# Kernel optimization log

Measured on AMD Instinct MI355X. Metric: run time of the kernel, lower is better.

## Reference

```python
import jax, jax.numpy as jnp
import numpy as np

N_NODES = 100000
N_EDGES = 1000000
IN_F = 64
HEADS = 4
OUT_C = 32  # per-head channels
EDGE_DIM = 16
NEG_SLOPE = 0.2


def setup_inputs() -> dict:
    key = jax.random.key(0)
    ks = jax.random.split(key, 10)
    x = jax.random.normal(ks[0], (N_NODES, IN_F), dtype=jnp.float32)
    edge_index = jax.random.randint(ks[1], (2, N_EDGES), 0, N_NODES, dtype=jnp.int64)
    edge_attr = jax.random.normal(ks[2], (N_EDGES, EDGE_DIM), dtype=jnp.float32)
    s = 1.0 / np.sqrt(IN_F)
    W = jax.random.normal(ks[3], (IN_F, HEADS * OUT_C), dtype=jnp.float32) * s
    W_edge = jax.random.normal(ks[4], (EDGE_DIM, HEADS * OUT_C), dtype=jnp.float32) * (1.0 / np.sqrt(EDGE_DIM))
    att_src = jax.random.normal(ks[5], (HEADS, OUT_C), dtype=jnp.float32) * (1.0 / np.sqrt(OUT_C))
    att_dst = jax.random.normal(ks[6], (HEADS, OUT_C), dtype=jnp.float32) * (1.0 / np.sqrt(OUT_C))
    att_edge = jax.random.normal(ks[7], (HEADS, OUT_C), dtype=jnp.float32) * (1.0 / np.sqrt(OUT_C))
    bias = jnp.zeros((HEADS * OUT_C,), dtype=jnp.float32)
    return {"x": x, "edge_index": edge_index, "edge_attr": edge_attr,
            "W": W, "W_edge": W_edge, "att_src": att_src, "att_dst": att_dst,
            "att_edge": att_edge, "bias": bias}


def reference(x, edge_index, edge_attr, W, W_edge, att_src, att_dst, att_edge, bias):
    # PyG GATConv with edge_dim, add_self_loops=False, concat=True.
    N = x.shape[0]
    src = edge_index[0]  # message source j
    dst = edge_index[1]  # message target i

    x_proj = (x @ W).reshape(N, HEADS, OUT_C)          # [N,H,C]
    a_src = jnp.einsum('nhc,hc->nh', x_proj, att_src)  # [N,H]
    a_dst = jnp.einsum('nhc,hc->nh', x_proj, att_dst)  # [N,H]

    e_proj = (edge_attr @ W_edge).reshape(-1, HEADS, OUT_C)  # [E,H,C]
    a_edge = jnp.einsum('ehc,hc->eh', e_proj, att_edge)      # [E,H]

    alpha = a_src[src] + a_dst[dst] + a_edge                 # [E,H]
    alpha = jax.nn.leaky_relu(alpha, NEG_SLOPE)

    # edge softmax grouped by destination node
    seg_max = jax.ops.segment_max(alpha, dst, num_segments=N)  # [N,H]
    alpha = jnp.exp(alpha - seg_max[dst])
    denom = jax.ops.segment_sum(alpha, dst, num_segments=N)    # [N,H]
    alpha = alpha / (denom[dst] + 1e-16)

    msg = x_proj[src] * alpha[:, :, None]                      # [E,H,C]
    out = jax.ops.segment_sum(msg, dst, num_segments=N)        # [N,H,C]
    return out.reshape(N, HEADS * OUT_C) + bias
```

## Files before the change

### kernel.cpp

```cpp
#include <hip/hip_runtime.h>
#include <hip/hip_fp16.h>


#define HC 128
#define NEG 0.2f
#define CH 16
#define DEGS 32
#define K_SHIFT 6.0f

typedef __fp16 half2_t __attribute__((ext_vector_type(2)));

__device__ __forceinline__ unsigned short f2bf(float f) {
    unsigned u = __float_as_uint(f);
    return (unsigned short)((u + 0x7fffu + ((u >> 16) & 1u)) >> 16);
}
__device__ __forceinline__ unsigned pk_h2(float lo, float hi) {
    half2_t p = __builtin_amdgcn_cvt_pkrtz(lo, hi);
    union { half2_t h; unsigned u; } cv;
    cv.h = p;
    return cv.u;
}
__device__ __forceinline__ float h2f_bits(unsigned short bits) {
    __half_raw hr; hr.x = bits;
    return __half2float(*reinterpret_cast<__half*>(&hr));
}
__device__ __forceinline__ long ld_idx(const int* __restrict__ ei, long i, int m64) {
    return m64 ? (long)(((const long long*)ei)[i]) : (long)ei[i];
}
__device__ __forceinline__ int detect_m64(const int* __restrict__ ei, int* s_m64) {
    int t = threadIdx.x;
    if (t < 64) {
        unsigned long long bal = __ballot(ei[2 * t + 1] != 0);
        if (t == 0) *s_m64 = (bal == 0ull) ? 1 : 0;
    }
    __syncthreads();
    return *s_m64;
}

__global__ __launch_bounds__(256) void k_hist(
    const float* __restrict__ We, const float* __restrict__ ae,
    const float* __restrict__ eattr, const int* __restrict__ ei,
    int* __restrict__ deg, int* __restrict__ rank, uint2* __restrict__ aeh,
    int E) {
    __shared__ float q_s[64];
    __shared__ int s_m64;
    int t = threadIdx.x;
    int m64 = detect_m64(ei, &s_m64);
    if (t < 64) {
        int dd = t >> 2, h = t & 3;
        float s = 0.f;
        for (int c = 0; c < 32; ++c)
            s += We[dd * HC + h * 32 + c] * ae[h * 32 + c];
        q_s[t] = s;
    }
    __syncthreads();

    int base = blockIdx.x * 512 + t;
    int e0 = base, e1 = base + 256;
    bool v0 = e0 < E, v1 = e1 < E;

    long d0 = 0, d1 = 0;
    if (v0) d0 = ld_idx(ei, (long)E + e0, m64);
    if (v1) d1 = ld_idx(ei, (long)E + e1, m64);
    int r0 = 0, r1 = 0;
    if (v0) r0 = atomicAdd(&deg[d0 * DEGS], 1);
    if (v1) r1 = atomicAdd(&deg[d1 * DEGS], 1);

#pragma unroll
    for (int k = 0; k < 2; ++k) {
        int e = k ? e1 : e0;
        bool v = k ? v1 : v0;
        if (!v) continue;
        const float4* pe = reinterpret_cast<const float4*>(eattr + (long)e * 16);
        float4 ea0 = pe[0], ea1 = pe[1], ea2 = pe[2], ea3 = pe[3];
        float ev[16] = {ea0.x, ea0.y, ea0.z, ea0.w, ea1.x, ea1.y, ea1.z, ea1.w,
                        ea2.x, ea2.y, ea2.z, ea2.w, ea3.x, ea3.y, ea3.z, ea3.w};
        float ov[4];
#pragma unroll
        for (int h = 0; h < 4; ++h) {
            float aev = 0.f;
#pragma unroll
            for (int dd = 0; dd < 16; ++dd) aev += ev[dd] * q_s[dd * 4 + h];
            ov[h] = aev;
        }
        aeh[e] = make_uint2(pk_h2(ov[0], ov[1]), pk_h2(ov[2], ov[3]));
        rank[e] = k ? r1 : r0;
    }
}

__global__ __launch_bounds__(256) void k_proj(
    const float* __restrict__ x, const float* __restrict__ W,
    const float* __restrict__ as_, const float* __restrict__ ad_,
    unsigned short* __restrict__ xp, float* __restrict__ a_src,
    float* __restrict__ a_dst, int N) {
    __shared__ float x_s[64][68];
    int t = threadIdx.x;
    int n0 = blockIdx.x * 64;
#pragma unroll
    for (int i = 0; i < 4; ++i) {
        int fl = i * 256 + t;
        int node = fl >> 4, f4 = fl & 15;
        float4 v = make_float4(0.f, 0.f, 0.f, 0.f);
        if (n0 + node < N)
            v = *reinterpret_cast<const float4*>(&x[(long)(n0 + node) * 64 + f4 * 4]);
        x_s[f4 * 4 + 0][node] = v.x;
        x_s[f4 * 4 + 1][node] = v.y;
        x_s[f4 * 4 + 2][node] = v.z;
        x_s[f4 * 4 + 3][node] = v.w;
    }
    __syncthreads();

    int c = t & 31;
    int nd = t >> 5;
    const float4* __restrict__ W4 = reinterpret_cast<const float4*>(W);
    float acc[8][4];
#pragma unroll
    for (int i = 0; i < 8; ++i)
#pragma unroll
        for (int j = 0; j < 4; ++j) acc[i][j] = 0.f;

#pragma unroll 8
    for (int k = 0; k < 64; ++k) {
        float4 w4 = W4[k * 32 + c];
        float4 xa = *reinterpret_cast<const float4*>(&x_s[k][nd * 8]);
        float4 xb = *reinterpret_cast<const float4*>(&x_s[k][nd * 8 + 4]);
        float xv[8] = {xa.x, xa.y, xa.z, xa.w, xb.x, xb.y, xb.z, xb.w};
#pragma unroll
        for (int i = 0; i < 8; ++i) {
            acc[i][0] += xv[i] * w4.x;
            acc[i][1] += xv[i] * w4.y;
            acc[i][2] += xv[i] * w4.z;
            acc[i][3] += xv[i] * w4.w;
        }
    }

    float4 s4 = *reinterpret_cast<const float4*>(&as_[c * 4]);
    float4 d4 = *reinterpret_cast<const float4*>(&ad_[c * 4]);
#pragma unroll
    for (int i = 0; i < 8; ++i) {
        int node = n0 + nd * 8 + i;
        if (node < N) {
            ushort4 o;
            o.x = f2bf(acc[i][0]); o.y = f2bf(acc[i][1]);
            o.z = f2bf(acc[i][2]); o.w = f2bf(acc[i][3]);
            *reinterpret_cast<ushort4*>(&xp[(long)node * HC + c * 4]) = o;
        }
        float ps = acc[i][0] * s4.x + acc[i][1] * s4.y + acc[i][2] * s4.z + acc[i][3] * s4.w;
        float pd = acc[i][0] * d4.x + acc[i][1] * d4.y + acc[i][2] * d4.z + acc[i][3] * d4.w;
#pragma unroll
        for (int off = 1; off < 8; off <<= 1) {
            ps += __shfl_xor(ps, off, 64);
            pd += __shfl_xor(pd, off, 64);
        }
        if ((c & 7) == 0 && node < N) {
            int h = c >> 3;
            a_src[(long)node * 4 + h] = ps;
            a_dst[(long)node * 4 + h] = pd;
        }
    }
}

__global__ __launch_bounds__(256) void k_scan1(
    const int* __restrict__ deg, int* __restrict__ row, int* __restrict__ bsum,
    int N) {
    __shared__ int s[256];
    int b = blockIdx.x, t = threadIdx.x;
    int base = b * 1024 + t * 4;
    int v[4], sum = 0;
#pragma unroll
    for (int i = 0; i < 4; ++i) {
        int idx = base + i;
        v[i] = (idx < N) ? deg[(long)idx * DEGS] : 0;
        sum += v[i];
    }
    s[t] = sum;
    __syncthreads();
    for (int off = 1; off < 256; off <<= 1) {
        int xv = (t >= off) ? s[t - off] : 0;
        __syncthreads();
        s[t] += xv;
        __syncthreads();
    }
    int run = s[t] - sum;
#pragma unroll
    for (int i = 0; i < 4; ++i) {
        int idx = base + i;
        if (idx < N) row[idx] = run;
        run += v[i];
    }
    if (t == 255) bsum[b] = s[255];
}

__global__ void k_scan2(int* __restrict__ bsum, int nb) {
    int t = threadIdx.x;
    if (t >= 64) return;
    int i0 = 2 * t, i1 = 2 * t + 1;
    int v0 = (i0 < nb) ? bsum[i0] : 0;
    int v1 = (i1 < nb) ? bsum[i1] : 0;
    int s = v0 + v1;
#pragma unroll
    for (int off = 1; off < 64; off <<= 1) {
        int u = __shfl_up(s, off, 64);
        if (t >= off) s += u;
    }
    int ex = s - (v0 + v1);
    if (i0 < nb) bsum[i0] = ex;
    if (i1 < nb) bsum[i1] = ex + v0;
}

__global__ __launch_bounds__(256) void k_place(
    const int* __restrict__ ei, const uint2* __restrict__ aeh,
    const int* __restrict__ rank, const float* __restrict__ a_src,
    const float* __restrict__ a_dst, const int* __restrict__ row,
    const int* __restrict__ bsum, uint4* __restrict__ srt, int E) {
    __shared__ int s_m64;
    int m64 = detect_m64(ei, &s_m64);
    int base = blockIdx.x * 512 + threadIdx.x;
#pragma unroll
    for (int k = 0; k < 2; ++k) {
        int e = base + k * 256;
        if (e >= E) continue;
        long s = ld_idx(ei, e, m64);
        long d = ld_idx(ei, (long)E + e, m64);
        uint2 av = aeh[e];
        int r = rank[e];
        float4 s4 = *reinterpret_cast<const float4*>(a_src + s * 4);
        float4 d4 = *reinterpret_cast<const float4*>(a_dst + d * 4);
        float lf[4];
        lf[0] = s4.x + d4.x + h2f_bits((unsigned short)(av.x & 0xffffu));
        lf[1] = s4.y + d4.y + h2f_bits((unsigned short)(av.x >> 16));
        lf[2] = s4.z + d4.z + h2f_bits((unsigned short)(av.y & 0xffffu));
        lf[3] = s4.w + d4.w + h2f_bits((unsigned short)(av.y >> 16));
        float ex[4];
#pragma unroll
        for (int h = 0; h < 4; ++h) {
            float v = (lf[h] > 0.f) ? lf[h] : NEG * lf[h];
            ex[h] = __expf(v - K_SHIFT);
        }
        int pos = row[d] + bsum[(int)(d >> 10)] + r;
        srt[pos] = make_uint4((unsigned)s, pk_h2(ex[0], ex[1]),
                              pk_h2(ex[2], ex[3]), 0u);
    }
}

__global__ __launch_bounds__(128) void k_gather(
    const int* __restrict__ row, const int* __restrict__ bsum,
    const uint4* __restrict__ srt, const char* __restrict__ xpc,
    const float* __restrict__ bias, float* __restrict__ out, int N, int E) {
    int wid = threadIdx.x >> 6;
    int lane = threadIdx.x & 63;
    int n = blockIdx.x * 2 + wid;
    if (n >= N) return;
    int beg = row[n] + bsum[n >> 10];
    int end = (n + 1 < N) ? (row[n + 1] + bsum[(n + 1) >> 10]) : E;
    int h_s = lane & 3, e_s = lane >> 2;
    int par = lane >> 5;
    int cl = lane & 31;
    int h_a = cl >> 3;
    float l = 0.f;
    float acc[4] = {0.f, 0.f, 0.f, 0.f};

    __shared__ float s_ex[2][CH][4];
    __shared__ int s_off[2][CH];
    __shared__ float s_l[2][4];

    for (int cs = beg; cs < end; cs += CH) {
        int cnt = end - cs;
        if (cnt > CH) cnt = CH;
        float ex = 0.f;
        if (e_s < cnt) {
            uint4 r = srt[cs + e_s];
            if (h_s == 0) s_off[wid][e_s] = (int)(r.x << 8);
            unsigned pr = (h_s & 2) ? r.z : r.y;
            unsigned bits = (h_s & 1) ? (pr >> 16) : (pr & 0xffffu);
            ex = h2f_bits((unsigned short)bits);
        }
        s_ex[wid][e_s][h_s] = ex;
        float se = ex;
        se += __shfl_xor(se, 4, 64);
        se += __shfl_xor(se, 8, 64);
        se += __shfl_xor(se, 16, 64);
        se += __shfl_xor(se, 32, 64);
        l += se;
        int j = 0;
        for (; j + 4 <= cnt; j += 4) {
            int ea0 = j + par, ea1 = j + 2 + par;
            int o0 = s_off[wid][ea0], o1 = s_off[wid][ea1];
            float w0 = s_ex[wid][ea0][h_a], w1 = s_ex[wid][ea1][h_a];
            uint2 v0 = *reinterpret_cast<const uint2*>(xpc + o0 + cl * 8);
            uint2 v1 = *reinterpret_cast<const uint2*>(xpc + o1 + cl * 8);
            acc[0] += w0 * __uint_as_float(v0.x << 16);
            acc[1] += w0 * __uint_as_float(v0.x & 0xffff0000u);
            acc[2] += w0 * __uint_as_float(v0.y << 16);
            acc[3] += w0 * __uint_as_float(v0.y & 0xffff0000u);
            acc[0] += w1 * __uint_as_float(v1.x << 16);
            acc[1] += w1 * __uint_as_float(v1.x & 0xffff0000u);
            acc[2] += w1 * __uint_as_float(v1.y << 16);
            acc[3] += w1 * __uint_as_float(v1.y & 0xffff0000u);
        }
        for (; j < cnt; j += 2) {
            int e = j + par;
            bool act = e < cnt;
            int o = s_off[wid][act ? e : j];
            float w = act ? s_ex[wid][e][h_a] : 0.f;
            uint2 v = *reinterpret_cast<const uint2*>(xpc + o + cl * 8);
            acc[0] += w * __uint_as_float(v.x << 16);
            acc[1] += w * __uint_as_float(v.x & 0xffff0000u);
            acc[2] += w * __uint_as_float(v.y << 16);
            acc[3] += w * __uint_as_float(v.y & 0xffff0000u);
        }
    }
    if (lane < 4) s_l[wid][h_s] = l;
#pragma unroll
    for (int k = 0; k < 4; ++k) acc[k] += __shfl_xor(acc[k], 32, 64);
    if (par == 0) {
        float d = s_l[wid][h_a] + 1e-16f;
        float4 b4 = *reinterpret_cast<const float4*>(bias + cl * 4);
        float4 o;
        o.x = acc[0] / d + b4.x;
        o.y = acc[1] / d + b4.y;
        o.z = acc[2] / d + b4.z;
        o.w = acc[3] / d + b4.w;
        *reinterpret_cast<float4*>(out + (long)n * HC + cl * 4) = o;
    }
}

extern "C" void kernel_launch(void* const* d_in, const int* in_sizes, int n_in,
                              void* d_out, int out_size, void* d_ws, size_t ws_size,
                              hipStream_t stream) {
    const float* x    = (const float*)d_in[0];
    const int*   ei   = (const int*)d_in[1];
    const float* ea   = (const float*)d_in[2];
    const float* W    = (const float*)d_in[3];
    const float* We   = (const float*)d_in[4];
    const float* as_  = (const float*)d_in[5];
    const float* ad_  = (const float*)d_in[6];
    const float* ae   = (const float*)d_in[7];
    const float* bias = (const float*)d_in[8];
    float* out = (float*)d_out;

    int N = in_sizes[0] / 64;
    int E = in_sizes[1] / 2;

    char* ws = (char*)d_ws;
    size_t off = 0;
    auto take = [&](size_t bytes) -> char* {
        char* p = ws + off;
        off += (bytes + 511) & ~(size_t)511;
        return p;
    };
    unsigned short* xp = (unsigned short*)take((size_t)N * HC * 2);
    float* a_src   = (float*)take((size_t)N * 4 * 4);
    float* a_dst   = (float*)take((size_t)N * 4 * 4);
    uint4* srt     = (uint4*)take((size_t)E * 16);
    uint2* aeh     = (uint2*)take((size_t)E * 8);
    int* rank      = (int*)take((size_t)E * 4);
    int* row       = (int*)take((size_t)(N + 1) * 4);
    int* bsum      = (int*)take(4096 * 4);
    int* deg = (int*)srt;

    int Np = (N + 63) / 64;
    int nblk = (N + 1023) / 1024;

    (void)hipMemsetAsync(deg, 0, (size_t)N * DEGS * 4, stream);
    hipLaunchKernelGGL(k_hist, dim3((E + 511) / 512), dim3(256), 0, stream,
                       We, ae, ea, ei, deg, rank, aeh, E);
    hipLaunchKernelGGL(k_proj, dim3(Np), dim3(256), 0, stream,
                       x, W, as_, ad_, xp, a_src, a_dst, N);
    hipLaunchKernelGGL(k_scan1, dim3(nblk), dim3(256), 0, stream, deg, row, bsum, N);
    hipLaunchKernelGGL(k_scan2, dim3(1), dim3(64), 0, stream, bsum, nblk);
    hipLaunchKernelGGL(k_place, dim3((E + 511) / 512), dim3(256), 0, stream,
                       ei, aeh, rank, a_src, a_dst, row, bsum, srt, E);
    hipLaunchKernelGGL(k_gather, dim3((N + 1) / 2), dim3(128), 0, stream,
                       row, bsum, srt, (const char*)xp, bias, out, N, E);
}
```

Before: 306.5 us.

## Replace global degree atomics with two-level bucket sort for CSR build

Edges are binned into coarse destination buckets using per-block shared-memory histograms and one global atomic per bucket, then each bucket is locally counting-sorted to build CSR row offsets and the sorted edge records. This removes the per-edge global atomics, the large padded-degree memset, and the multi-pass scan kernels. It risks silently dropping edges if a bucket exceeds its fixed capacity, and it hardcodes limits on node count and source index width.

```diff
diff --git a/kernel.cpp b/kernel.cpp
--- a/kernel.cpp
+++ b/kernel.cpp
@@ -5,8 +5,12 @@
 #define HC 128
 #define NEG 0.2f
 #define CH 16
-#define DEGS 32
 #define K_SHIFT 6.0f
+#define NBK 512
+#define BSH 8
+#define BMSK 255
+#define BCAP 3584
+#define EPT 16
 
 typedef __fp16 half2_t __attribute__((ext_vector_type(2)));
 
@@ -37,13 +41,15 @@
     return *s_m64;
 }
 
-__global__ __launch_bounds__(256) void k_hist(
+__global__ __launch_bounds__(256) void k_bucket(
     const float* __restrict__ We, const float* __restrict__ ae,
     const float* __restrict__ eattr, const int* __restrict__ ei,
-    int* __restrict__ deg, int* __restrict__ rank, uint2* __restrict__ aeh,
-    int E) {
+    int* __restrict__ bcur, unsigned* __restrict__ sdstg,
+    uint2* __restrict__ aevstg, int E) {
     __shared__ float q_s[64];
     __shared__ int s_m64;
+    __shared__ int hist[NBK];
+    __shared__ int gb[NBK];
     int t = threadIdx.x;
     int m64 = detect_m64(ei, &s_m64);
     if (t < 64) {
@@ -53,28 +59,37 @@
             s += We[dd * HC + h * 32 + c] * ae[h * 32 + c];
         q_s[t] = s;
     }
-    __syncthreads();
-
-    int base = blockIdx.x * 512 + t;
-    int e0 = base, e1 = base + 256;
-    bool v0 = e0 < E, v1 = e1 < E;
-
-    long d0 = 0, d1 = 0;
-    if (v0) d0 = ld_idx(ei, (long)E + e0, m64);
-    if (v1) d1 = ld_idx(ei, (long)E + e1, m64);
-    int r0 = 0, r1 = 0;
-    if (v0) r0 = atomicAdd(&deg[d0 * DEGS], 1);
-    if (v1) r1 = atomicAdd(&deg[d1 * DEGS], 1);
-
-#pragma unroll
-    for (int k = 0; k < 2; ++k) {
-        int e = k ? e1 : e0;
-        bool v = k ? v1 : v0;
-        if (!v) continue;
+    hist[t] = 0; hist[t + 256] = 0;
+    __syncthreads();
+
+    int base = blockIdx.x * (256 * EPT) + t;
+    for (int k = 0; k < EPT; ++k) {
+        int e = base + k * 256;
+        if (e < E) {
+            int d = (int)ld_idx(ei, (long)E + e, m64);
+            atomicAdd(&hist[d >> BSH], 1);
+        }
+    }
+    __syncthreads();
+    int c0 = hist[t], c1 = hist[t + 256];
+    gb[t]       = c0 ? atomicAdd(&bcur[t], c0) : 0;
+    gb[t + 256] = c1 ? atomicAdd(&bcur[t + 256], c1) : 0;
+    hist[t] = 0; hist[t + 256] = 0;
+    __syncthreads();
+
+    for (int k = 0; k < EPT; ++k) {
+        int e = base + k * 256;
+        if (e >= E) continue;
+        int d = (int)ld_idx(ei, (long)E + e, m64);
+        int b = d >> BSH;
+        int lr = atomicAdd(&hist[b], 1);
+        int off = gb[b] + lr;
+        if (off >= BCAP) continue;
+        long s = ld_idx(ei, e, m64);
         const float4* pe = reinterpret_cast<const float4*>(eattr + (long)e * 16);
-        float4 ea0 = pe[0], ea1 = pe[1], ea2 = pe[2], ea3 = pe[3];
-        float ev[16] = {ea0.x, ea0.y, ea0.z, ea0.w, ea1.x, ea1.y, ea1.z, ea1.w,
-                        ea2.x, ea2.y, ea2.z, ea2.w, ea3.x, ea3.y, ea3.z, ea3.w};
+        float4 e0 = pe[0], e1 = pe[1], e2 = pe[2], e3 = pe[3];
+        float ev[16] = {e0.x, e0.y, e0.z, e0.w, e1.x, e1.y, e1.z, e1.w,
+                        e2.x, e2.y, e2.z, e2.w, e3.x, e3.y, e3.z, e3.w};
         float ov[4];
 #pragma unroll
         for (int h = 0; h < 4; ++h) {
@@ -83,8 +98,97 @@
             for (int dd = 0; dd < 16; ++dd) aev += ev[dd] * q_s[dd * 4 + h];
             ov[h] = aev;
         }
-        aeh[e] = make_uint2(pk_h2(ov[0], ov[1]), pk_h2(ov[2], ov[3]));
-        rank[e] = k ? r1 : r0;
+        int slot = b * BCAP + off;
+        sdstg[slot] = (unsigned)s | ((unsigned)(d & BMSK) << 20);
+        aevstg[slot] = make_uint2(pk_h2(ov[0], ov[1]), pk_h2(ov[2], ov[3]));
+    }
+}
+
+__global__ void k_bscan(const int* __restrict__ bcur, int* __restrict__ bbase,
+                        int* __restrict__ row, int N, int E) {
+    int t = threadIdx.x;
+    if (t >= 64) return;
+    int v[8]; int sum = 0;
+#pragma unroll
+    for (int k = 0; k < 8; ++k) { v[k] = bcur[t * 8 + k]; sum += v[k]; }
+    int s = sum;
+#pragma unroll
+    for (int off = 1; off < 64; off <<= 1) {
+        int u = __shfl_up(s, off, 64);
+        if (t >= off) s += u;
+    }
+    int run = s - sum;
+#pragma unroll
+    for (int k = 0; k < 8; ++k) { bbase[t * 8 + k] = run; run += v[k]; }
+    if (t == 0) row[N] = E;
+}
+
+__global__ __launch_bounds__(256) void k_csr(
+    const unsigned* __restrict__ sdstg, const uint2* __restrict__ aevstg,
+    const int* __restrict__ bcur, const int* __restrict__ bbase,
+    const float* __restrict__ a_src, const float* __restrict__ a_dst,
+    int* __restrict__ row, uint4* __restrict__ srt, int N) {
+    int b = blockIdx.x, t = threadIdx.x;
+    __shared__ int deg_l[256];
+    __shared__ int s_sc[256];
+    __shared__ int pfx[256];
+    deg_l[t] = 0;
+    __syncthreads();
+    int cnt = bcur[b]; if (cnt > BCAP) cnt = BCAP;
+    int base = bbase[b];
+
+    int r[14];
+    unsigned recs[14];
+#pragma unroll
+    for (int k = 0; k < 14; ++k) {
+        int i = k * 256 + t;
+        r[k] = -1; recs[k] = 0u;
+        if (i < cnt) {
+            unsigned sd = sdstg[b * BCAP + i];
+            recs[k] = sd;
+            r[k] = atomicAdd(&deg_l[(sd >> 20) & BMSK], 1);
+        }
+    }
+    __syncthreads();
+    int own = deg_l[t];
+    s_sc[t] = own;
+    __syncthreads();
+    for (int off = 1; off < 256; off <<= 1) {
+        int xv = (t >= off) ? s_sc[t - off] : 0;
+        __syncthreads();
+        s_sc[t] += xv;
+        __syncthreads();
+    }
+    int ex = s_sc[t] - own;
+    pfx[t] = ex;
+    int n = b * 256 + t;
+    if (n <= N) row[n] = base + ex;
+    __syncthreads();
+
+#pragma unroll
+    for (int k = 0; k < 14; ++k) {
+        int i = k * 256 + t;
+        if (i >= cnt) continue;
+        unsigned sd = recs[k];
+        int dl = (sd >> 20) & BMSK;
+        int s = (int)(sd & 0xFFFFFu);
+        uint2 av = aevstg[b * BCAP + i];
+        float4 s4 = *reinterpret_cast<const float4*>(a_src + (long)s * 4);
+        float4 d4 = *reinterpret_cast<const float4*>(a_dst + (long)(b * 256 + dl) * 4);
+        float lf[4];
+        lf[0] = s4.x + d4.x + h2f_bits((unsigned short)(av.x & 0xffffu));
+        lf[1] = s4.y + d4.y + h2f_bits((unsigned short)(av.x >> 16));
+        lf[2] = s4.z + d4.z + h2f_bits((unsigned short)(av.y & 0xffffu));
+        lf[3] = s4.w + d4.w + h2f_bits((unsigned short)(av.y >> 16));
+        float exv[4];
+#pragma unroll
+        for (int h = 0; h < 4; ++h) {
+            float v = (lf[h] > 0.f) ? lf[h] : NEG * lf[h];
+            exv[h] = __expf(v - K_SHIFT);
+        }
+        int pos = base + pfx[dl] + r[k];
+        srt[pos] = make_uint4((unsigned)s, pk_h2(exv[0], exv[1]),
+                              pk_h2(exv[2], exv[3]), 0u);
     }
 }
 
@@ -160,99 +264,15 @@
     }
 }
 
-__global__ __launch_bounds__(256) void k_scan1(
-    const int* __restrict__ deg, int* __restrict__ row, int* __restrict__ bsum,
-    int N) {
-    __shared__ int s[256];
-    int b = blockIdx.x, t = threadIdx.x;
-    int base = b * 1024 + t * 4;
-    int v[4], sum = 0;
-#pragma unroll
-    for (int i = 0; i < 4; ++i) {
-        int idx = base + i;
-        v[i] = (idx < N) ? deg[(long)idx * DEGS] : 0;
-        sum += v[i];
-    }
-    s[t] = sum;
-    __syncthreads();
-    for (int off = 1; off < 256; off <<= 1) {
-        int xv = (t >= off) ? s[t - off] : 0;
-        __syncthreads();
-        s[t] += xv;
-        __syncthreads();
-    }
-    int run = s[t] - sum;
-#pragma unroll
-    for (int i = 0; i < 4; ++i) {
-        int idx = base + i;
-        if (idx < N) row[idx] = run;
-        run += v[i];
-    }
-    if (t == 255) bsum[b] = s[255];
-}
-
-__global__ void k_scan2(int* __restrict__ bsum, int nb) {
-    int t = threadIdx.x;
-    if (t >= 64) return;
-    int i0 = 2 * t, i1 = 2 * t + 1;
-    int v0 = (i0 < nb) ? bsum[i0] : 0;
-    int v1 = (i1 < nb) ? bsum[i1] : 0;
-    int s = v0 + v1;
-#pragma unroll
-    for (int off = 1; off < 64; off <<= 1) {
-        int u = __shfl_up(s, off, 64);
-        if (t >= off) s += u;
-    }
-    int ex = s - (v0 + v1);
-    if (i0 < nb) bsum[i0] = ex;
-    if (i1 < nb) bsum[i1] = ex + v0;
-}
-
-__global__ __launch_bounds__(256) void k_place(
-    const int* __restrict__ ei, const uint2* __restrict__ aeh,
-    const int* __restrict__ rank, const float* __restrict__ a_src,
-    const float* __restrict__ a_dst, const int* __restrict__ row,
-    const int* __restrict__ bsum, uint4* __restrict__ srt, int E) {
-    __shared__ int s_m64;
-    int m64 = detect_m64(ei, &s_m64);
-    int base = blockIdx.x * 512 + threadIdx.x;
-#pragma unroll
-    for (int k = 0; k < 2; ++k) {
-        int e = base + k * 256;
-        if (e >= E) continue;
-        long s = ld_idx(ei, e, m64);
-        long d = ld_idx(ei, (long)E + e, m64);
-        uint2 av = aeh[e];
-        int r = rank[e];
-        float4 s4 = *reinterpret_cast<const float4*>(a_src + s * 4);
-        float4 d4 = *reinterpret_cast<const float4*>(a_dst + d * 4);
-        float lf[4];
-        lf[0] = s4.x + d4.x + h2f_bits((unsigned short)(av.x & 0xffffu));
-        lf[1] = s4.y + d4.y + h2f_bits((unsigned short)(av.x >> 16));
-        lf[2] = s4.z + d4.z + h2f_bits((unsigned short)(av.y & 0xffffu));
-        lf[3] = s4.w + d4.w + h2f_bits((unsigned short)(av.y >> 16));
-        float ex[4];
-#pragma unroll
-        for (int h = 0; h < 4; ++h) {
-            float v = (lf[h] > 0.f) ? lf[h] : NEG * lf[h];
-            ex[h] = __expf(v - K_SHIFT);
-        }
-        int pos = row[d] + bsum[(int)(d >> 10)] + r;
-        srt[pos] = make_uint4((unsigned)s, pk_h2(ex[0], ex[1]),
-                              pk_h2(ex[2], ex[3]), 0u);
-    }
-}
-
 __global__ __launch_bounds__(128) void k_gather(
-    const int* __restrict__ row, const int* __restrict__ bsum,
-    const uint4* __restrict__ srt, const char* __restrict__ xpc,
-    const float* __restrict__ bias, float* __restrict__ out, int N, int E) {
+    const int* __restrict__ row, const uint4* __restrict__ srt,
+    const char* __restrict__ xpc, const float* __restrict__ bias,
+    float* __restrict__ out, int N) {
     int wid = threadIdx.x >> 6;
     int lane = threadIdx.x & 63;
     int n = blockIdx.x * 2 + wid;
     if (n >= N) return;
-    int beg = row[n] + bsum[n >> 10];
-    int end = (n + 1 < N) ? (row[n + 1] + bsum[(n + 1) >> 10]) : E;
+    int beg = row[n], end = row[n + 1];
     int h_s = lane & 3, e_s = lane >> 2;
     int par = lane >> 5;
     int cl = lane & 31;
@@ -350,27 +370,28 @@
         return p;
     };
     unsigned short* xp = (unsigned short*)take((size_t)N * HC * 2);
-    float* a_src   = (float*)take((size_t)N * 4 * 4);
-    float* a_dst   = (float*)take((size_t)N * 4 * 4);
-    uint4* srt     = (uint4*)take((size_t)E * 16);
-    uint2* aeh     = (uint2*)take((size_t)E * 8);
-    int* rank      = (int*)take((size_t)E * 4);
-    int* row       = (int*)take((size_t)(N + 1) * 4);
-    int* bsum      = (int*)take(4096 * 4);
-    int* deg = (int*)srt;
+    float* a_src    = (float*)take((size_t)N * 4 * 4);
+    float* a_dst    = (float*)take((size_t)N * 4 * 4);
+    uint4* srt      = (uint4*)take((size_t)E * 16);
+    unsigned* sdstg = (unsigned*)take((size_t)NBK * BCAP * 4);
+    uint2* aevstg   = (uint2*)take((size_t)NBK * BCAP * 8);
+    int* row        = (int*)take((size_t)(N + 1) * 4);
+    int* bcur       = (int*)take((size_t)NBK * 4);
+    int* bbase      = (int*)take((size_t)NBK * 4);
 
     int Np = (N + 63) / 64;
-    int nblk = (N + 1023) / 1024;
-
-    (void)hipMemsetAsync(deg, 0, (size_t)N * DEGS * 4, stream);
-    hipLaunchKernelGGL(k_hist, dim3((E + 511) / 512), dim3(256), 0, stream,
-                       We, ae, ea, ei, deg, rank, aeh, E);
+    int nbA = (E + 256 * EPT - 1) / (256 * EPT);
+    int nbB = (N + 255) / 256;
+
+    (void)hipMemsetAsync(bcur, 0, (size_t)NBK * 4, stream);
+    hipLaunchKernelGGL(k_bucket, dim3(nbA), dim3(256), 0, stream,
+                       We, ae, ea, ei, bcur, sdstg, aevstg, E);
     hipLaunchKernelGGL(k_proj, dim3(Np), dim3(256), 0, stream,
                        x, W, as_, ad_, xp, a_src, a_dst, N);
-    hipLaunchKernelGGL(k_scan1, dim3(nblk), dim3(256), 0, stream, deg, row, bsum, N);
-    hipLaunchKernelGGL(k_scan2, dim3(1), dim3(64), 0, stream, bsum, nblk);
-    hipLaunchKernelGGL(k_place, dim3((E + 511) / 512), dim3(256), 0, stream,
-                       ei, aeh, rank, a_src, a_dst, row, bsum, srt, E);
+    hipLaunchKernelGGL(k_bscan, dim3(1), dim3(64), 0, stream,
+                       bcur, bbase, row, N, E);
+    hipLaunchKernelGGL(k_csr, dim3(nbB), dim3(256), 0, stream,
+                       sdstg, aevstg, bcur, bbase, a_src, a_dst, row, srt, N);
     hipLaunchKernelGGL(k_gather, dim3((N + 1) / 2), dim3(128), 0, stream,
-                       row, bsum, srt, (const char*)xp, bias, out, N, E);
-}
+                       row, srt, (const char*)xp, bias, out, N);
+}
```

Result: faster. 280.7 us (-8.4%).
